# Performance work log

Measured on AMD Instinct MI355X. Metric: run time of the kernel, lower is better.

Reference implementation:

```python
import jax, jax.numpy as jnp
import numpy as np

C = 128   # d_pair, fixed by the fp8 tri-mul kernel assert
H = 128   # d_hidden


def layer_norm(x, w, b, eps=1e-5):
    m = jnp.mean(x, axis=-1, keepdims=True)
    v = jnp.mean(jnp.square(x - m), axis=-1, keepdims=True)
    return (x - m) * jax.lax.rsqrt(v + eps) * w + b


def setup_inputs() -> dict:
    key = jax.random.key(0)
    ks = jax.random.split(key, 12)
    B, N = 1, 512
    s_in = 1.0 / np.sqrt(C)
    s_h = 1.0 / np.sqrt(H)
    return {
        "z": jax.random.normal(ks[0], (B, N, N, C), jnp.float32),
        "mask": jnp.ones((B, N, N), jnp.float32),
        "ln_in_w": jnp.ones((C,), jnp.float32),
        "ln_in_b": jnp.zeros((C,), jnp.float32),
        "w_ap": jax.random.normal(ks[1], (C, H), jnp.float32) * s_in,
        "b_ap": jnp.zeros((H,), jnp.float32),
        "w_ag": jax.random.normal(ks[2], (C, H), jnp.float32) * s_in,
        "b_ag": jnp.zeros((H,), jnp.float32),
        "w_bp": jax.random.normal(ks[3], (C, H), jnp.float32) * s_in,
        "b_bp": jnp.zeros((H,), jnp.float32),
        "w_bg": jax.random.normal(ks[4], (C, H), jnp.float32) * s_in,
        "b_bg": jnp.zeros((H,), jnp.float32),
        "ln_out_w": jnp.ones((H,), jnp.float32),
        "ln_out_b": jnp.zeros((H,), jnp.float32),
        "w_o": jax.random.normal(ks[5], (H, C), jnp.float32) * s_h,
        "b_o": jnp.zeros((C,), jnp.float32),
        "w_g": jax.random.normal(ks[6], (C, C), jnp.float32) * s_in,
        "b_g": jnp.zeros((C,), jnp.float32),
    }


def reference(z, mask, ln_in_w, ln_in_b, w_ap, b_ap, w_ag, b_ag,
              w_bp, b_bp, w_bg, b_bg, ln_out_w, ln_out_b, w_o, b_o, w_g, b_g):
    # Triangular multiplicative update (outgoing), gated projections.
    z_ln = layer_norm(z, ln_in_w, ln_in_b)                      # [B,N,N,C]
    m = mask[..., None]                                         # [B,N,N,1]
    a = m * jax.nn.sigmoid(z_ln @ w_ag + b_ag) * (z_ln @ w_ap + b_ap)
    b = m * jax.nn.sigmoid(z_ln @ w_bg + b_bg) * (z_ln @ w_bp + b_bp)
    # outgoing: x[b,i,j,c] = sum_k a[b,i,k,c] * b[b,j,k,c]
    x = jnp.einsum("bikc,bjkc->bijc", a, b)                     # [B,N,N,H]
    x = layer_norm(x, ln_out_w, ln_out_b)
    g = jax.nn.sigmoid(z_ln @ w_g + b_g)                        # output gate
    return g * (x @ w_o + b_o)
```

## Files before the change

kernel.cpp:

```cpp
#include <hip/hip_runtime.h>
#include <hip/hip_bf16.h>
#include <stdint.h>

#define NDIM 512
#define NN (NDIM*NDIM)
#define CDIM 128
#define LDSP 136

typedef __attribute__((ext_vector_type(8))) short short8;
typedef __attribute__((ext_vector_type(4))) short short4v;
typedef __attribute__((ext_vector_type(4))) float f32x4;

__device__ __forceinline__ unsigned short f2bf(float f) {
    union { float f; uint32_t u; } v; v.f = f;
    uint32_t u = v.u;
    return (unsigned short)((u + 0x7FFFu + ((u >> 16) & 1u)) >> 16);
}
__device__ __forceinline__ float bf2f(unsigned short b) {
    union { uint32_t u; float f; } v; v.u = ((uint32_t)b) << 16;
    return v.f;
}
__device__ __forceinline__ f32x4 mfma16(short8 a, short8 b, f32x4 c) {
    return __builtin_amdgcn_mfma_f32_16x16x32_bf16(a, b, c, 0, 0, 0);
}
__device__ __forceinline__ void gl_lds16(const void* g, void* l) {
    __builtin_amdgcn_global_load_lds((const __attribute__((address_space(1))) void*)g,
                                     (__attribute__((address_space(3))) void*)l,
                                     16, 0, 0);
}

__global__ void k0_prep(const float* __restrict__ w_ag, const float* __restrict__ w_ap,
                        const float* __restrict__ w_bg, const float* __restrict__ w_bp,
                        const float* __restrict__ w_g,  const float* __restrict__ w_o,
                        unsigned short* __restrict__ Wcat, unsigned short* __restrict__ Wo_t)
{
    int idx = blockIdx.x * 256 + threadIdx.x;
    if (idx < 640*128) {
        int col = idx >> 7, k = idx & 127;
        int s = col >> 7, h = col & 127;
        const float* w = (s==0) ? w_ag : (s==1) ? w_ap : (s==2) ? w_bg : (s==3) ? w_bp : w_g;
        Wcat[idx] = f2bf(w[k*128 + h]);
    } else if (idx < 640*128 + 128*128) {
        int i2 = idx - 640*128;
        int cc = i2 >> 7, h = i2 & 127;
        Wo_t[i2] = f2bf(w_o[h*128 + cc]);
    }
}

__global__ __launch_bounds__(256, 2) void k1_proj(
    const float* __restrict__ z, const float* __restrict__ mask,
    const float* __restrict__ lnw, const float* __restrict__ lnb,
    const unsigned short* __restrict__ Wcat,
    const float* __restrict__ b_ag, const float* __restrict__ b_ap,
    const float* __restrict__ b_bg, const float* __restrict__ b_bp,
    const float* __restrict__ b_g,
    unsigned short* __restrict__ a_t, unsigned short* __restrict__ b_t,
    unsigned short* __restrict__ g_out)
{
    __shared__ unsigned short zb[128*LDSP];
    __shared__ unsigned short wb[128*LDSP];
    __shared__ float mask_s[128];
    __shared__ float lnw_s[128];
    __shared__ float lnb_s[128];
    __shared__ float bias_s[640];

    const int t = threadIdx.x;
    const int pos0 = blockIdx.x * 128;
    const int tid2 = t >> 1, half = t & 1;
    const int wave = t >> 6, lane = t & 63;
    const int lr = lane & 15, lh = lane >> 4;

    if (t < 128) {
        lnw_s[t] = lnw[t];
        lnb_s[t] = lnb[t];
        mask_s[t] = mask[pos0 + t];
    }
    for (int i = t; i < 640; i += 256) {
        int s = i >> 7, c = i & 127;
        const float* bp = (s==0) ? b_ag : (s==1) ? b_ap : (s==2) ? b_bg : (s==3) ? b_bp : b_g;
        bias_s[i] = bp[c];
    }

    float v[64];
    float s0 = 0.f, s1 = 0.f;
    {
        const float* zr = z + (size_t)(pos0 + tid2) * CDIM + half * 64;
        #pragma unroll
        for (int i = 0; i < 16; i++) {
            float4 q = *(const float4*)(zr + i*4);
            v[i*4+0] = q.x; v[i*4+1] = q.y; v[i*4+2] = q.z; v[i*4+3] = q.w;
        }
        #pragma unroll
        for (int i = 0; i < 64; i++) { s0 += v[i]; s1 += v[i]*v[i]; }
        s0 += __shfl_xor(s0, 1);
        s1 += __shfl_xor(s1, 1);
    }
    __syncthreads();
    {
        float m  = s0 * (1.f/128.f);
        float va = s1 * (1.f/128.f) - m*m;
        float rs = rsqrtf(va + 1e-5f);
        #pragma unroll
        for (int i = 0; i < 64; i++) {
            int c = half*64 + i;
            zb[tid2*LDSP + c] = f2bf((v[i]-m)*rs*lnw_s[c] + lnb_s[c]);
        }
    }

    f32x4 aG[2][8], aP[2][8];

    auto zero2 = [&](f32x4 (&acc)[2][8]) {
        #pragma unroll
        for (int m = 0; m < 2; m++)
            #pragma unroll
            for (int n = 0; n < 8; n++) { f32x4 zz = {0.f,0.f,0.f,0.f}; acc[m][n] = zz; }
    };
    auto load_w = [&](int s) {
        const unsigned short* src = Wcat + ((size_t)(s*128 + tid2) * 128 + half*64);
        unsigned short* dst = wb + tid2*LDSP + half*64;
        #pragma unroll
        for (int i = 0; i < 8; i++)
            *(short8*)(dst + i*8) = *(const short8*)(src + i*8);
    };
    auto gemm = [&](f32x4 (&acc)[2][8]) {
        #pragma unroll
        for (int kk = 0; kk < 4; kk++) {
            const int k0 = kk*32 + lh*8;
            short8 af0 = *(const short8*)&zb[(wave*32 + lr)*LDSP + k0];
            short8 af1 = *(const short8*)&zb[(wave*32 + 16 + lr)*LDSP + k0];
            #pragma unroll
            for (int n = 0; n < 8; n++) {
                short8 bf = *(const short8*)&wb[(n*16 + lr)*LDSP + k0];
                acc[0][n] = mfma16(af0, bf, acc[0][n]);
                acc[1][n] = mfma16(af1, bf, acc[1][n]);
            }
        }
    };
    auto store_trans = [&](unsigned short* dstg) {
        const unsigned short* src = wb + tid2*LDSP + half*64;
        unsigned short* dst = dstg + (size_t)tid2*NN + pos0 + half*64;
        #pragma unroll
        for (int i = 0; i < 8; i++)
            *(short8*)(dst + i*8) = *(const short8*)(src + i*8);
    };
    auto epi_pair = [&](int boffG, int boffP, unsigned short* dstg) {
        #pragma unroll
        for (int m = 0; m < 2; m++) {
            int rb = wave*32 + m*16 + lh*4;
            #pragma unroll
            for (int n = 0; n < 8; n++) {
                int col = n*16 + lr;
                float bgv = bias_s[boffG + col];
                float bpv = bias_s[boffP + col];
                short4v pk;
                #pragma unroll
                for (int r = 0; r < 4; r++) {
                    float gate = 1.f / (1.f + __expf(-(aG[m][n][r] + bgv)));
                    float proj = aP[m][n][r] + bpv;
                    pk[r] = (short)f2bf(mask_s[rb + r] * gate * proj);
                }
                *(short4v*)&wb[col*LDSP + rb] = pk;
            }
        }
        __syncthreads();
        store_trans(dstg);
        __syncthreads();
    };

    load_w(0);
    __syncthreads();
    zero2(aG); gemm(aG);
    __syncthreads();
    load_w(1); __syncthreads();
    zero2(aP); gemm(aP);
    __syncthreads();
    epi_pair(0, 128, a_t);

    load_w(2); __syncthreads();
    zero2(aG); gemm(aG);
    __syncthreads();
    load_w(3); __syncthreads();
    zero2(aP); gemm(aP);
    __syncthreads();
    epi_pair(256, 384, b_t);

    load_w(4); __syncthreads();
    zero2(aG); gemm(aG);
    __syncthreads();
    #pragma unroll
    for (int m = 0; m < 2; m++) {
        int rb = wave*32 + m*16 + lh*4;
        #pragma unroll
        for (int n = 0; n < 8; n++) {
            int col = n*16 + lr;
            float bb = bias_s[512 + col];
            #pragma unroll
            for (int r = 0; r < 4; r++) {
                float val = 1.f / (1.f + __expf(-(aG[m][n][r] + bb)));
                wb[(rb + r)*LDSP + col] = f2bf(val);
            }
        }
    }
    __syncthreads();
    {
        const unsigned short* src = wb + tid2*LDSP + half*64;
        unsigned short* dst = g_out + (size_t)(pos0 + tid2)*CDIM + half*64;
        #pragma unroll
        for (int i = 0; i < 8; i++)
            *(short8*)(dst + i*8) = *(const short8*)(src + i*8);
    }
}

__global__ __launch_bounds__(256, 2) void k2_einsum(
    const unsigned short* __restrict__ a_t,
    const unsigned short* __restrict__ b_t,
    unsigned short* __restrict__ x_t)
{
    __shared__ unsigned short As[128*64];
    __shared__ unsigned short Bs[128*64];

    const int c  = blockIdx.y;
    const int ti = (blockIdx.x >> 2) * 128;
    const int tj = (blockIdx.x & 3) * 128;
    const int t = threadIdx.x;
    const int wave = t >> 6, lane = t & 63;
    const int lr = lane & 15, lh = lane >> 4;
    const int wm = wave >> 1, wn = wave & 1;

    const unsigned short* Ag = a_t + (size_t)c*NN + (size_t)ti*NDIM;
    const unsigned short* Bg = b_t + (size_t)c*NN + (size_t)tj*NDIM;

    const int srow = wave*32 + (lane >> 3);
    const int scol = (lane & 7) * 8;

    f32x4 acc[4][4] = {};

    for (int k0 = 0; k0 < NDIM; k0 += 64) {
        __syncthreads();
        #pragma unroll
        for (int it = 0; it < 4; it++) {
            int r = srow + it*8;
            gl_lds16(Ag + (size_t)r*NDIM + k0 + scol, (void*)(As + (wave*32 + it*8)*64));
            gl_lds16(Bg + (size_t)r*NDIM + k0 + scol, (void*)(Bs + (wave*32 + it*8)*64));
        }
        asm volatile("s_waitcnt vmcnt(0)" ::: "memory");
        __syncthreads();
        #pragma unroll
        for (int kk = 0; kk < 2; kk++) {
            const int kof = kk*32 + lh*8;
            short8 af[4], bfr[4];
            #pragma unroll
            for (int m = 0; m < 4; m++)
                af[m] = *(const short8*)&As[(wm*64 + m*16 + lr)*64 + kof];
            #pragma unroll
            for (int n = 0; n < 4; n++)
                bfr[n] = *(const short8*)&Bs[(wn*64 + n*16 + lr)*64 + kof];
            #pragma unroll
            for (int m = 0; m < 4; m++)
                #pragma unroll
                for (int n = 0; n < 4; n++)
                    acc[m][n] = mfma16(af[m], bfr[n], acc[m][n]);
        }
    }

    #pragma unroll
    for (int m = 0; m < 4; m++) {
        int row = ti + wm*64 + m*16 + lh*4;
        #pragma unroll
        for (int n = 0; n < 4; n++) {
            int col = tj + wn*64 + n*16 + lr;
            unsigned short* dst = x_t + (size_t)c*NN + (size_t)row*NDIM + col;
            #pragma unroll
            for (int r = 0; r < 4; r++)
                dst[(size_t)r*NDIM] = f2bf(acc[m][n][r]);
        }
    }
}

__global__ __launch_bounds__(256, 2) void k3_out(
    const unsigned short* __restrict__ x_t,
    const unsigned short* __restrict__ g_in,
    const unsigned short* __restrict__ Wo_t,
    const float* __restrict__ lnw, const float* __restrict__ lnb,
    const float* __restrict__ b_o,
    float* __restrict__ out)
{
    __shared__ unsigned short xb[128*LDSP];
    __shared__ unsigned short zl[128*LDSP];
    __shared__ float lnw_s[128];
    __shared__ float lnb_s[128];
    __shared__ float bo_s[128];

    const int t = threadIdx.x;
    const int pos0 = blockIdx.x * 128;
    const int tid2 = t >> 1, half = t & 1;
    const int wave = t >> 6, lane = t & 63;
    const int lr = lane & 15, lh = lane >> 4;

    if (t < 128) { lnw_s[t] = lnw[t]; lnb_s[t] = lnb[t]; bo_s[t] = b_o[t]; }

    {
        const unsigned short* src = x_t + (size_t)tid2*NN + pos0 + half*64;
        unsigned short* dst = xb + tid2*LDSP + half*64;
        #pragma unroll
        for (int i = 0; i < 8; i++)
            *(short8*)(dst + i*8) = *(const short8*)(src + i*8);
    }
    __syncthreads();

    {
        float v[64];
        float s0 = 0.f, s1 = 0.f;
        #pragma unroll
        for (int i = 0; i < 64; i++) {
            float x = bf2f(xb[(half*64 + i)*LDSP + tid2]);
            v[i] = x; s0 += x; s1 += x*x;
        }
        s0 += __shfl_xor(s0, 1);
        s1 += __shfl_xor(s1, 1);
        float m  = s0 * (1.f/128.f);
        float va = s1 * (1.f/128.f) - m*m;
        float rs = rsqrtf(va + 1e-5f);
        #pragma unroll
        for (int i = 0; i < 64; i++) {
            int cc = half*64 + i;
            zl[tid2*LDSP + cc] = f2bf((v[i]-m)*rs*lnw_s[cc] + lnb_s[cc]);
        }
    }
    __syncthreads();

    {
        const unsigned short* src = Wo_t + ((size_t)tid2*128 + half*64);
        unsigned short* dst = xb + tid2*LDSP + half*64;
        #pragma unroll
        for (int i = 0; i < 8; i++)
            *(short8*)(dst + i*8) = *(const short8*)(src + i*8);
    }
    __syncthreads();

    f32x4 acc[2][8];
    #pragma unroll
    for (int m = 0; m < 2; m++)
        #pragma unroll
        for (int n = 0; n < 8; n++) { f32x4 zz = {0.f,0.f,0.f,0.f}; acc[m][n] = zz; }

    #pragma unroll
    for (int kk = 0; kk < 4; kk++) {
        const int k0 = kk*32 + lh*8;
        short8 af0 = *(const short8*)&zl[(wave*32 + lr)*LDSP + k0];
        short8 af1 = *(const short8*)&zl[(wave*32 + 16 + lr)*LDSP + k0];
        #pragma unroll
        for (int n = 0; n < 8; n++) {
            short8 bf = *(const short8*)&xb[(n*16 + lr)*LDSP + k0];
            acc[0][n] = mfma16(af0, bf, acc[0][n]);
            acc[1][n] = mfma16(af1, bf, acc[1][n]);
        }
    }
    __syncthreads();

    {
        const unsigned short* src = g_in + (size_t)(pos0 + tid2)*CDIM + half*64;
        unsigned short* dst = zl + tid2*LDSP + half*64;
        #pragma unroll
        for (int i = 0; i < 8; i++)
            *(short8*)(dst + i*8) = *(const short8*)(src + i*8);
    }
    __syncthreads();

    #pragma unroll
    for (int m = 0; m < 2; m++) {
        int rb = wave*32 + m*16 + lh*4;
        #pragma unroll
        for (int n = 0; n < 8; n++) {
            int col = n*16 + lr;
            float bo = bo_s[col];
            #pragma unroll
            for (int r = 0; r < 4; r++) {
                int row = rb + r;
                float gv = bf2f(zl[row*LDSP + col]);
                out[(size_t)(pos0 + row)*CDIM + col] = gv * (acc[m][n][r] + bo);
            }
        }
    }
}

extern "C" void kernel_launch(void* const* d_in, const int* in_sizes, int n_in,
                              void* d_out, int out_size, void* d_ws, size_t ws_size,
                              hipStream_t stream) {
    const float* z        = (const float*)d_in[0];
    const float* mask     = (const float*)d_in[1];
    const float* ln_in_w  = (const float*)d_in[2];
    const float* ln_in_b  = (const float*)d_in[3];
    const float* w_ap     = (const float*)d_in[4];
    const float* b_ap     = (const float*)d_in[5];
    const float* w_ag     = (const float*)d_in[6];
    const float* b_ag     = (const float*)d_in[7];
    const float* w_bp     = (const float*)d_in[8];
    const float* b_bp     = (const float*)d_in[9];
    const float* w_bg     = (const float*)d_in[10];
    const float* b_bg     = (const float*)d_in[11];
    const float* ln_out_w = (const float*)d_in[12];
    const float* ln_out_b = (const float*)d_in[13];
    const float* w_o      = (const float*)d_in[14];
    const float* b_o      = (const float*)d_in[15];
    const float* w_g      = (const float*)d_in[16];
    const float* b_g      = (const float*)d_in[17];

    char* ws = (char*)d_ws;
    const size_t BUF = (size_t)NN * 128 * 2;
    unsigned short* a_t  = (unsigned short*)(ws);
    unsigned short* b_t  = (unsigned short*)(ws + BUF);
    unsigned short* g_b  = (unsigned short*)(ws + 2*BUF);
    unsigned short* x_t  = (unsigned short*)(ws + 3*BUF);
    unsigned short* Wcat = (unsigned short*)(ws + 4*BUF);
    unsigned short* Wo_t = (unsigned short*)(ws + 4*BUF + 640*128*2);

    k0_prep<<<384, 256, 0, stream>>>(w_ag, w_ap, w_bg, w_bp, w_g, w_o, Wcat, Wo_t);
    k1_proj<<<NN/128, 256, 0, stream>>>(z, mask, ln_in_w, ln_in_b, Wcat,
                                        b_ag, b_ap, b_bg, b_bp, b_g, a_t, b_t, g_b);
    k2_einsum<<<dim3(16, 128), 256, 0, stream>>>(a_t, b_t, x_t);
    k3_out<<<NN/128, 256, 0, stream>>>(x_t, g_b, Wo_t, ln_out_w, ln_out_b, b_o,
                                       (float*)d_out);
}
```

Baseline: 311.0 us.

## Read projection weights from global in k1, drop weight LDS tile, raise occupancy

The projection kernel no longer stages each 128x128 weight slice in shared memory. MFMA B fragments are read directly from global/L2 and the second LDS buffer is removed. Output columns are split into two 64-wide halves to shrink accumulator registers, and launch bounds are raised to four blocks per CU. The transposed a/b stores now go straight from registers as 4-element strided global writes instead of through an LDS transpose, which cuts barriers but gives poorly coalesced stores and repeated uncached-in-LDS weight loads.

New measurement: 392.1 us. 1.26x slower.

```diff
diff --git a/kernel.cpp b/kernel.cpp
--- a/kernel.cpp
+++ b/kernel.cpp
@@ -47,7 +47,7 @@
     }
 }
 
-__global__ __launch_bounds__(256, 2) void k1_proj(
+__global__ __launch_bounds__(256, 4) void k1_proj(
     const float* __restrict__ z, const float* __restrict__ mask,
     const float* __restrict__ lnw, const float* __restrict__ lnb,
     const unsigned short* __restrict__ Wcat,
@@ -58,7 +58,6 @@
     unsigned short* __restrict__ g_out)
 {
     __shared__ unsigned short zb[128*LDSP];
-    __shared__ unsigned short wb[128*LDSP];
     __shared__ float mask_s[128];
     __shared__ float lnw_s[128];
     __shared__ float lnb_s[128];
@@ -101,109 +100,93 @@
         float va = s1 * (1.f/128.f) - m*m;
         float rs = rsqrtf(va + 1e-5f);
         #pragma unroll
-        for (int i = 0; i < 64; i++) {
-            int c = half*64 + i;
-            zb[tid2*LDSP + c] = f2bf((v[i]-m)*rs*lnw_s[c] + lnb_s[c]);
-        }
-    }
-
-    f32x4 aG[2][8], aP[2][8];
-
-    auto zero2 = [&](f32x4 (&acc)[2][8]) {
+        for (int i = 0; i < 8; i++) {
+            short8 pk;
+            #pragma unroll
+            for (int j = 0; j < 8; j++) {
+                int c = half*64 + i*8 + j;
+                pk[j] = (short)f2bf((v[i*8+j]-m)*rs*lnw_s[c] + lnb_s[c]);
+            }
+            *(short8*)&zb[tid2*LDSP + half*64 + i*8] = pk;
+        }
+    }
+    __syncthreads();
+
+    const int rowA0 = (wave*32 + lr)*LDSP;
+    const int rowA1 = (wave*32 + 16 + lr)*LDSP;
+
+    auto gemmh = [&](int s, int h, f32x4 (&acc)[2][4]) {
         #pragma unroll
         for (int m = 0; m < 2; m++)
             #pragma unroll
-            for (int n = 0; n < 8; n++) { f32x4 zz = {0.f,0.f,0.f,0.f}; acc[m][n] = zz; }
-    };
-    auto load_w = [&](int s) {
-        const unsigned short* src = Wcat + ((size_t)(s*128 + tid2) * 128 + half*64);
-        unsigned short* dst = wb + tid2*LDSP + half*64;
-        #pragma unroll
-        for (int i = 0; i < 8; i++)
-            *(short8*)(dst + i*8) = *(const short8*)(src + i*8);
-    };
-    auto gemm = [&](f32x4 (&acc)[2][8]) {
+            for (int n = 0; n < 4; n++) { f32x4 zz = {0.f,0.f,0.f,0.f}; acc[m][n] = zz; }
         #pragma unroll
         for (int kk = 0; kk < 4; kk++) {
             const int k0 = kk*32 + lh*8;
-            short8 af0 = *(const short8*)&zb[(wave*32 + lr)*LDSP + k0];
-            short8 af1 = *(const short8*)&zb[(wave*32 + 16 + lr)*LDSP + k0];
-            #pragma unroll
-            for (int n = 0; n < 8; n++) {
-                short8 bf = *(const short8*)&wb[(n*16 + lr)*LDSP + k0];
+            short8 af0 = *(const short8*)&zb[rowA0 + k0];
+            short8 af1 = *(const short8*)&zb[rowA1 + k0];
+            #pragma unroll
+            for (int n = 0; n < 4; n++) {
+                int col = h*64 + n*16 + lr;
+                short8 bf = *(const short8*)&Wcat[(size_t)(s*128 + col)*128 + k0];
                 acc[0][n] = mfma16(af0, bf, acc[0][n]);
                 acc[1][n] = mfma16(af1, bf, acc[1][n]);
             }
         }
     };
-    auto store_trans = [&](unsigned short* dstg) {
-        const unsigned short* src = wb + tid2*LDSP + half*64;
-        unsigned short* dst = dstg + (size_t)tid2*NN + pos0 + half*64;
-        #pragma unroll
-        for (int i = 0; i < 8; i++)
-            *(short8*)(dst + i*8) = *(const short8*)(src + i*8);
-    };
-    auto epi_pair = [&](int boffG, int boffP, unsigned short* dstg) {
+
+    auto pair_half = [&](int sG, int sP, int h, unsigned short* dstg) {
+        f32x4 G[2][4], P[2][4];
+        gemmh(sG, h, G);
+        gemmh(sP, h, P);
         #pragma unroll
         for (int m = 0; m < 2; m++) {
             int rb = wave*32 + m*16 + lh*4;
             #pragma unroll
-            for (int n = 0; n < 8; n++) {
-                int col = n*16 + lr;
-                float bgv = bias_s[boffG + col];
-                float bpv = bias_s[boffP + col];
+            for (int n = 0; n < 4; n++) {
+                int col = h*64 + n*16 + lr;
+                float bgv = bias_s[sG*128 + col];
+                float bpv = bias_s[sP*128 + col];
                 short4v pk;
                 #pragma unroll
                 for (int r = 0; r < 4; r++) {
-                    float gate = 1.f / (1.f + __expf(-(aG[m][n][r] + bgv)));
-                    float proj = aP[m][n][r] + bpv;
+                    float gate = 1.f / (1.f + __expf(-(G[m][n][r] + bgv)));
+                    float proj = P[m][n][r] + bpv;
                     pk[r] = (short)f2bf(mask_s[rb + r] * gate * proj);
                 }
-                *(short4v*)&wb[col*LDSP + rb] = pk;
+                *(short4v*)(dstg + (size_t)col*NN + pos0 + rb) = pk;
             }
         }
-        __syncthreads();
-        store_trans(dstg);
-        __syncthreads();
     };
 
-    load_w(0);
-    __syncthreads();
-    zero2(aG); gemm(aG);
-    __syncthreads();
-    load_w(1); __syncthreads();
-    zero2(aP); gemm(aP);
-    __syncthreads();
-    epi_pair(0, 128, a_t);
-
-    load_w(2); __syncthreads();
-    zero2(aG); gemm(aG);
-    __syncthreads();
-    load_w(3); __syncthreads();
-    zero2(aP); gemm(aP);
-    __syncthreads();
-    epi_pair(256, 384, b_t);
-
-    load_w(4); __syncthreads();
-    zero2(aG); gemm(aG);
+    pair_half(0, 1, 0, a_t);
+    pair_half(0, 1, 1, a_t);
+    pair_half(2, 3, 0, b_t);
+    pair_half(2, 3, 1, b_t);
+
+    f32x4 G0[2][4], G1[2][4];
+    gemmh(4, 0, G0);
+    gemmh(4, 1, G1);
     __syncthreads();
     #pragma unroll
     for (int m = 0; m < 2; m++) {
         int rb = wave*32 + m*16 + lh*4;
         #pragma unroll
-        for (int n = 0; n < 8; n++) {
-            int col = n*16 + lr;
-            float bb = bias_s[512 + col];
+        for (int n = 0; n < 4; n++) {
+            int c0 = n*16 + lr;
+            int c1 = 64 + n*16 + lr;
+            float b0 = bias_s[512 + c0];
+            float b1 = bias_s[512 + c1];
             #pragma unroll
             for (int r = 0; r < 4; r++) {
-                float val = 1.f / (1.f + __expf(-(aG[m][n][r] + bb)));
-                wb[(rb + r)*LDSP + col] = f2bf(val);
+                zb[(rb + r)*LDSP + c0] = f2bf(1.f / (1.f + __expf(-(G0[m][n][r] + b0))));
+                zb[(rb + r)*LDSP + c1] = f2bf(1.f / (1.f + __expf(-(G1[m][n][r] + b1))));
             }
         }
     }
     __syncthreads();
     {
-        const unsigned short* src = wb + tid2*LDSP + half*64;
+        const unsigned short* src = zb + tid2*LDSP + half*64;
         unsigned short* dst = g_out + (size_t)(pos0 + tid2)*CDIM + half*64;
         #pragma unroll
         for (int i = 0; i < 8; i++)
```
